# Performance work log

Hardware: AMD Instinct MI355X
Metric: run time of the kernel (lower is better)

The kernel has to match this reference:

```python
import math
import jax, jax.numpy as jnp
import numpy as np

B, S, D, H = 2, 4096, 512, 8
DH = D // H


def setup_inputs() -> dict:
    key = jax.random.key(0)
    ks = jax.random.split(key, 12)
    lim = 1.0 / math.sqrt(D)
    u = lambda k, shp: jax.random.uniform(k, shp, jnp.float32, -lim, lim)
    return {
        "x": jax.random.normal(ks[0], (B, S, D), jnp.float32),
        "gamma": jax.random.uniform(ks[1], (B, S, 1), jnp.float32),
        "Wq": u(ks[2], (D, D)), "bq": u(ks[3], (D,)),
        "Wk": u(ks[4], (D, D)), "bk": u(ks[5], (D,)),
        "Wv": u(ks[6], (D, D)), "bv": u(ks[7], (D,)),
        "Wo": u(ks[8], (D, D)), "bo": u(ks[9], (D,)),
    }


def reference(x, gamma, Wq, bq, Wk, bk, Wv, bv, Wo, bo):
    b, s, d = x.shape
    # projections (torch Linear: x @ W.T + b), split heads -> [B,H,S,DH]
    def proj(W, bias):
        return (x @ W.T + bias).reshape(b, s, H, DH).transpose(0, 2, 1, 3)
    q, k, v = proj(Wq, bq), proj(Wk, bk), proj(Wv, bv)

    scores = jnp.einsum("bhsd,bhtd->bhst", q, k) / math.sqrt(DH)  # [B,H,S,S]
    causal = jnp.triu(jnp.ones((s, s), bool), k=1)  # True above diagonal
    neg_inf = jnp.float32(-jnp.inf)
    scores = jnp.where(causal[None, None], neg_inf, scores)

    # hyperbolic positional bias: -log1p(gamma_i * max(i-j, 0) + 1e-8)
    pos = jnp.arange(s)
    delta = jnp.clip(pos[:, None] - pos[None, :], 0).astype(jnp.float32)  # [S,S]
    gamma_q = gamma[:, :, 0][:, :, None]  # [B,S,1]
    hyper = -jnp.log1p(gamma_q * delta + 1e-8)  # [B,S,S]
    hyper = jnp.where(causal[None], neg_inf, hyper)
    scores = scores + hyper[:, None]  # [B,H,S,S]

    attn = jax.nn.softmax(scores, axis=-1)
    out = jnp.einsum("bhst,bhtd->bhsd", attn, v)  # [B,H,S,DH]
    out = out.transpose(0, 2, 1, 3).reshape(b, s, d)
    return out @ Wo.T + bo
```

## Files before the change

### kernel.cpp

```cpp
#include <hip/hip_runtime.h>
#include <hip/hip_bf16.h>

#define Bb 2
#define Ss 4096
#define Dd 512
#define Hh 8
#define DHh 64

typedef __attribute__((ext_vector_type(8))) short short8;
typedef __attribute__((ext_vector_type(4))) float floatx4;

static __device__ __forceinline__ ushort bfbits(float f) {
  union { __hip_bfloat16 h; ushort u; } cv;
  cv.h = __float2bfloat16(f);
  return cv.u;
}

static __device__ __forceinline__ unsigned int packhi(float a, float b) {
  union { float f; unsigned int u; } ca, cb; ca.f = a; cb.f = b;
  return (ca.u >> 16) | (cb.u & 0xffff0000u);
}

__global__ void cvt_all(const float* __restrict__ x,
                        const float* __restrict__ w0, const float* __restrict__ w1,
                        const float* __restrict__ w2, const float* __restrict__ w3,
                        ushort* __restrict__ out) {
  const int XN4 = (Bb * Ss * Dd) / 4;
  const int WN4 = (Dd * Dd) / 4;
  int i = blockIdx.x * blockDim.x + threadIdx.x;
  if (i >= XN4 + 4 * WN4) return;
  const float* s; int li;
  if (i < XN4) { s = x; li = i; }
  else {
    int t = i - XN4; int j = t >> 16; li = t & (WN4 - 1);
    s = (j == 0) ? w0 : (j == 1) ? w1 : (j == 2) ? w2 : w3;
  }
  float4 f = ((const float4*)s)[li];
  ushort4 u;
  u.x = bfbits(f.x); u.y = bfbits(f.y); u.z = bfbits(f.z); u.w = bfbits(f.w);
  ((ushort4*)out)[i] = u;
}

static __device__ __forceinline__ int vperm(int s0) {
  int kb = (s0 >> 4) & 3, gq = (s0 >> 2) & 3;
  return (s0 & ~63) | ((kb >> 1) << 5) | (gq << 3) | ((kb & 1) << 2);
}

#define LDQK(buf, k0)                                                          \
  _Pragma("unroll")                                                            \
  for (int rb = 0; rb < 4; ++rb)                                               \
    af[buf][rb] = *(const short8*)(ap + (size_t)rb * 16 * 512 + (k0));         \
  _Pragma("unroll")                                                            \
  for (int cb = 0; cb < 4; ++cb)                                               \
    bf[buf][cb] = *(const short8*)(bp + (size_t)cb * 16 * 512 + (k0));

__global__ __launch_bounds__(256) void qkv_gemm(
    const ushort* __restrict__ xb,
    const ushort* __restrict__ Wq, const ushort* __restrict__ Wk, const ushort* __restrict__ Wv,
    const float* __restrict__ bq, const float* __restrict__ bk, const float* __restrict__ bv,
    ushort* __restrict__ qo, ushort* __restrict__ ko, ushort* __restrict__ vo)
{
  int mb = blockIdx.x / 12, rest = blockIdx.x % 12;
  int which = rest >> 2, nb = rest & 3;
  const ushort* Bw  = (which == 0) ? Wq : (which == 1) ? Wk : Wv;
  const float* bias = (which == 0) ? bq : (which == 1) ? bk : bv;
  int lane = threadIdx.x & 63, w = threadIdx.x >> 6;
  int wr = w & 1, wc = w >> 1;
  int g = lane >> 4, ln = lane & 15;
  int m0 = mb * 128 + wr * 64;
  int c0 = nb * 128 + wc * 64;
  const ushort* ap = xb + (size_t)(m0 + ln) * 512 + g * 8;
  const ushort* bp = Bw + (size_t)(c0 + ln) * 512 + g * 8;
  floatx4 acc[4][4] = {};
  short8 af[2][4], bf[2][4];
  LDQK(0, 0)
#pragma unroll
  for (int it = 0; it < 16; ++it) {
    int cur = it & 1;
    if (it < 15) { LDQK(cur ^ 1, (it + 1) * 32) }
#pragma unroll
    for (int rb = 0; rb < 4; ++rb)
#pragma unroll
      for (int cb = 0; cb < 4; ++cb)
        acc[rb][cb] = __builtin_amdgcn_mfma_f32_16x16x32_bf16(af[cur][rb], bf[cur][cb], acc[rb][cb], 0, 0, 0);
  }
  float scale = (which == 0) ? 0.18033688011112042f : 1.0f;
#pragma unroll
  for (int rb = 0; rb < 4; ++rb)
#pragma unroll
    for (int cb = 0; cb < 4; ++cb) {
      int col = c0 + cb * 16 + ln;
      float bv_ = bias[col];
      int hh = col >> 6, dh = col & 63;
      if (which == 2) {
        int i0 = m0 + rb * 16 + g * 4;
        int bI = i0 >> 12, s0 = i0 & (Ss - 1);
        ushort4 pk;
        pk.x = bfbits(acc[rb][cb][0] + bv_);
        pk.y = bfbits(acc[rb][cb][1] + bv_);
        pk.z = bfbits(acc[rb][cb][2] + bv_);
        pk.w = bfbits(acc[rb][cb][3] + bv_);
        *(ushort4*)(vo + (((size_t)bI * Hh + hh) * DHh + dh) * Ss + vperm(s0)) = pk;
      } else {
        ushort* outp = (which == 0) ? qo : ko;
#pragma unroll
        for (int r = 0; r < 4; ++r) {
          int i = m0 + rb * 16 + g * 4 + r;
          int bI = i >> 12, s = i & (Ss - 1);
          outp[(((size_t)bI * Hh + hh) * Ss + s) * DHh + dh] = bfbits((acc[rb][cb][r] + bv_) * scale);
        }
      }
    }
}

#define LD32(buf, k0)                                                          \
  af[buf][0] = *(const short8*)(ap + (k0));                                    \
  af[buf][1] = *(const short8*)(ap + 16 * 512 + (k0));                         \
  _Pragma("unroll")                                                            \
  for (int ns = 0; ns < 4; ++ns)                                               \
    bfr[buf][ns] = *(const short8*)(bp + (size_t)ns * 16 * 512 + (k0));

__global__ __launch_bounds__(256) void gemm_out(
    const ushort* __restrict__ A, const ushort* __restrict__ Bw,
    const float* __restrict__ bias, float* __restrict__ outp)
{
  int mb = blockIdx.x >> 3, nb = blockIdx.x & 7;
  int lane = threadIdx.x & 63, w = threadIdx.x >> 6;
  int g = lane >> 4, ln = lane & 15;
  int m0 = mb * 128 + w * 32;
  const ushort* ap = A + (size_t)(m0 + ln) * 512 + g * 8;
  const ushort* bp = Bw + (size_t)(nb * 64 + ln) * 512 + g * 8;
  floatx4 acc[2][4] = {};
  short8 af[2][2], bfr[2][4];
  LD32(0, 0)
#pragma unroll
  for (int it = 0; it < 16; ++it) {
    int cur = it & 1;
    if (it < 15) { LD32(cur ^ 1, (it + 1) * 32) }
#pragma unroll
    for (int ns = 0; ns < 4; ++ns) {
      acc[0][ns] = __builtin_amdgcn_mfma_f32_16x16x32_bf16(af[cur][0], bfr[cur][ns], acc[0][ns], 0, 0, 0);
      acc[1][ns] = __builtin_amdgcn_mfma_f32_16x16x32_bf16(af[cur][1], bfr[cur][ns], acc[1][ns], 0, 0, 0);
    }
  }
#pragma unroll
  for (int rb = 0; rb < 2; ++rb)
#pragma unroll
    for (int ns = 0; ns < 4; ++ns) {
      int col = nb * 64 + ns * 16 + ln;
      float bv_ = bias[col];
#pragma unroll
      for (int r = 0; r < 4; ++r)
        outp[(size_t)(m0 + rb * 16 + g * 4 + r) * 512 + col] = acc[rb][ns][r] + bv_;
    }
}

__global__ __launch_bounds__(192, 3) void flash13(
    const ushort* __restrict__ q, const ushort* __restrict__ k,
    const ushort* __restrict__ vt, const float* __restrict__ gamma,
    ushort* __restrict__ o)
{
  __shared__ __align__(16) float Pmrg[2][64][34];
  __shared__ __align__(16) ushort Tb[16 * 72];

  int z = blockIdx.x;
  int bh = z & 15;
  int b = bh >> 3, hh = bh & 7;
  int qsel = (z >> 4) & 1;
  int up = z >> 5;

  int tid = threadIdx.x;
  int wv = tid >> 6, lane = tid & 63;
  int g = lane >> 4, ln = lane & 15;

  const ushort* kp = k + ((size_t)bh * Ss + ln) * DHh + g * 8;
  const ushort* vp = vt + ((size_t)bh * DHh + ln) * Ss + g * 8;

#pragma unroll 1
  for (int rep = 0; rep < 2; ++rep) {
    int u = rep ? (63 - up) : up;
    int nkt = u + 1;
    int ktm = u;
    int qd = nkt / 3, rr = nkt % 3;
    int lo = wv * qd + (wv < rr ? wv : rr);
    int hi = lo + qd + (wv < rr ? 1 : 0);
    int q0 = (2 * u + qsel) * 32;

    const ushort* qp = q + ((size_t)bh * Ss + q0 + ln) * DHh + g * 8;
    short8 qf00 = *(const short8*)qp;
    short8 qf01 = *(const short8*)(qp + 32);
    short8 qf10 = *(const short8*)(qp + 16 * DHh);
    short8 qf11 = *(const short8*)(qp + 16 * DHh + 32);

    int qrow0 = q0 + ln, qrow1 = q0 + 16 + ln;
    float gm0 = gamma[(size_t)b * Ss + qrow0];
    float gm1 = gamma[(size_t)b * Ss + qrow1];
    float l2[2] = {0.0f, 0.0f};
    floatx4 oacc[2][4] = {};

    if (lo < hi) {
      short8 kfl[4], kfh[4];
      int kb0 = lo * 64;
#pragma unroll
      for (int ns = 0; ns < 4; ++ns) {
        kfl[ns] = *(const short8*)(kp + (size_t)(kb0 + ns * 16) * DHh);
        kfh[ns] = *(const short8*)(kp + (size_t)(kb0 + ns * 16) * DHh + 32);
      }

      for (int kt = lo; kt < hi; ++kt) {
        int kbase = kt * 64;
        bool last = (kt == ktm);
        short8 pfrag[2][2];
#pragma unroll
        for (int qb = 0; qb < 2; ++qb) {
          short8 qlo = qb ? qf10 : qf00;
          short8 qhi = qb ? qf11 : qf01;
          int qrow = qb ? qrow1 : qrow0;
          float gm = qb ? gm1 : gm0;
          int db = qrow - kbase - g * 4;
          float fd = (float)db;
          float base = fmaf(gm, fd, 1.0f);
#pragma unroll
          for (int nsg = 0; nsg < 2; ++nsg) {
            floatx4 za = {}, zb = {};
            za = __builtin_amdgcn_mfma_f32_16x16x32_bf16(kfl[2 * nsg + 0], qlo, za, 0, 0, 0);
            za = __builtin_amdgcn_mfma_f32_16x16x32_bf16(kfh[2 * nsg + 0], qhi, za, 0, 0, 0);
            zb = __builtin_amdgcn_mfma_f32_16x16x32_bf16(kfl[2 * nsg + 1], qlo, zb, 0, 0, 0);
            zb = __builtin_amdgcn_mfma_f32_16x16x32_bf16(kfh[2 * nsg + 1], qhi, zb, 0, 0, 0);
            float f[8];
#pragma unroll
            for (int r = 0; r < 4; ++r) { f[r] = za[r]; f[4 + r] = zb[r]; }
            float rs0 = 0.0f, rs1 = 0.0f;
            if (last) {
#pragma unroll
              for (int e = 0; e < 8; ++e) {
                int off = nsg * 32 + (e >> 2) * 16 + (e & 3);
                if (db - off < 0) f[e] = -1e30f;
                float delta = fmaxf(fd - (float)off, 0.0f);
                float wt = __builtin_amdgcn_rcpf(fmaf(gm, delta, 1.0f));
                float pv = __builtin_amdgcn_exp2f(f[e]) * wt;
                if (e & 1) rs1 += pv; else rs0 += pv;
                f[e] = pv;
              }
            } else {
#pragma unroll
              for (int e = 0; e < 8; ++e) {
                float off = (float)(nsg * 32 + (e >> 2) * 16 + (e & 3));
                float wt = __builtin_amdgcn_rcpf(fmaf(gm, -off, base));
                float pv = __builtin_amdgcn_exp2f(f[e]) * wt;
                if (e & 1) rs1 += pv; else rs0 += pv;
                f[e] = pv;
              }
            }
            l2[qb] += rs0 + rs1;
            uint4 pkd;
            pkd.x = packhi(f[0], f[1]);
            pkd.y = packhi(f[2], f[3]);
            pkd.z = packhi(f[4], f[5]);
            pkd.w = packhi(f[6], f[7]);
            pfrag[qb][nsg] = *(short8*)&pkd;
          }
        }
        if (kt + 1 < hi) {
          const ushort* kn = kp + (size_t)(kbase + 64) * DHh;
#pragma unroll
          for (int ns = 0; ns < 4; ++ns) {
            kfl[ns] = *(const short8*)(kn + (size_t)(ns * 16) * DHh);
            kfh[ns] = *(const short8*)(kn + (size_t)(ns * 16) * DHh + 32);
          }
        }
#pragma unroll
        for (int c = 0; c < 2; ++c) {
          short8 vfg[4];
#pragma unroll
          for (int ds = 0; ds < 4; ++ds)
            vfg[ds] = *(const short8*)(vp + (size_t)(ds * 16) * Ss + kbase + c * 32);
#pragma unroll
          for (int ds = 0; ds < 4; ++ds) {
            oacc[0][ds] = __builtin_amdgcn_mfma_f32_16x16x32_bf16(vfg[ds], pfrag[0][c], oacc[0][ds], 0, 0, 0);
            oacc[1][ds] = __builtin_amdgcn_mfma_f32_16x16x32_bf16(vfg[ds], pfrag[1][c], oacc[1][ds], 0, 0, 0);
          }
        }
      }
    }

    if (wv) {
#pragma unroll
      for (int qb = 0; qb < 2; ++qb)
#pragma unroll
        for (int ds = 0; ds < 4; ++ds)
#pragma unroll
          for (int r = 0; r < 4; ++r)
            Pmrg[wv - 1][lane][qb * 16 + ds * 4 + r] = oacc[qb][ds][r];
      Pmrg[wv - 1][lane][32] = l2[0];
      Pmrg[wv - 1][lane][33] = l2[1];
    }
    __syncthreads();
    if (wv == 0) {
#pragma unroll
      for (int qb = 0; qb < 2; ++qb) {
#pragma unroll
        for (int ds = 0; ds < 4; ++ds)
#pragma unroll
          for (int r = 0; r < 4; ++r)
            oacc[qb][ds][r] += Pmrg[0][lane][qb * 16 + ds * 4 + r]
                             + Pmrg[1][lane][qb * 16 + ds * 4 + r];
        float l = l2[qb] + Pmrg[0][lane][32 + qb] + Pmrg[1][lane][32 + qb];
        l += __shfl_xor(l, 16);
        l += __shfl_xor(l, 32);
        float linv = 1.0f / l;
        ushort* tb = &Tb[0];
#pragma unroll
        for (int ds = 0; ds < 4; ++ds)
#pragma unroll
          for (int r = 0; r < 4; ++r)
            tb[ln * 72 + ds * 16 + g * 4 + r] = bfbits(oacc[qb][ds][r] * linv);
        short8 v0 = *(const short8*)(tb + ln * 72 + g * 16);
        short8 v1 = *(const short8*)(tb + ln * 72 + g * 16 + 8);
        size_t oa = ((size_t)b * Ss + q0 + qb * 16 + ln) * Dd + hh * DHh + g * 16;
        *(short8*)(o + oa) = v0;
        *(short8*)(o + oa + 8) = v1;
      }
    }
    __syncthreads();
  }
}

extern "C" void kernel_launch(void* const* d_in, const int* in_sizes, int n_in,
                              void* d_out, int out_size, void* d_ws, size_t ws_size,
                              hipStream_t stream) {
  const float* x     = (const float*)d_in[0];
  const float* gamma = (const float*)d_in[1];
  const float* Wq    = (const float*)d_in[2];
  const float* bq    = (const float*)d_in[3];
  const float* Wk    = (const float*)d_in[4];
  const float* bk    = (const float*)d_in[5];
  const float* Wv    = (const float*)d_in[6];
  const float* bv    = (const float*)d_in[7];
  const float* Wo    = (const float*)d_in[8];
  const float* bo    = (const float*)d_in[9];

  const size_t NX = (size_t)Bb * Ss * Dd;
  const size_t NW = (size_t)Dd * Dd;
  ushort* xb  = (ushort*)d_ws;
  ushort* Wqb = xb + NX;
  ushort* Wkb = Wqb + NW;
  ushort* Wvb = Wkb + NW;
  ushort* Wob = Wvb + NW;
  ushort* qb  = Wob + NW;
  ushort* kb  = qb + NX;
  ushort* vtb = kb + NX;
  ushort* ab  = vtb + NX;

  const int total4 = (int)(NX / 4 + 4 * (NW / 4));
  cvt_all<<<(total4 + 255) / 256, 256, 0, stream>>>(x, Wq, Wk, Wv, Wo, xb);

  qkv_gemm<<<64 * 12, 256, 0, stream>>>(xb, Wqb, Wkb, Wvb, bq, bk, bv, qb, kb, vtb);

  flash13<<<1024, 192, 0, stream>>>(qb, kb, vtb, gamma, ab);

  gemm_out<<<512, 256, 0, stream>>>(ab, Wob, bo, (float*)d_out);
}
```

Baseline: 294.6 us.

## Shrink QKV GEMM tiles to one head per block and relax flash launch bounds

The QKV projection now assigns each block a 128-row by 64-column tile covering one head, with each of the four waves computing 32x64 instead of 64x64. The grid doubles to 1536 blocks for more parallelism and fewer registers per wave, at the cost of more redundant global loads of the weight tiles. The attention kernel also drops its min-blocks-per-CU hint, which lets the compiler use more registers but may lower occupancy.

```diff
diff --git a/kernel.cpp b/kernel.cpp
--- a/kernel.cpp
+++ b/kernel.cpp
@@ -46,10 +46,9 @@
   return (s0 & ~63) | ((kb >> 1) << 5) | (gq << 3) | ((kb & 1) << 2);
 }
 
-#define LDQK(buf, k0)                                                          \
-  _Pragma("unroll")                                                            \
-  for (int rb = 0; rb < 4; ++rb)                                               \
-    af[buf][rb] = *(const short8*)(ap + (size_t)rb * 16 * 512 + (k0));         \
+#define LDH(buf, k0)                                                           \
+  af[buf][0] = *(const short8*)(ap + (k0));                                    \
+  af[buf][1] = *(const short8*)(ap + 16 * 512 + (k0));                         \
   _Pragma("unroll")                                                            \
   for (int cb = 0; cb < 4; ++cb)                                               \
     bf[buf][cb] = *(const short8*)(bp + (size_t)cb * 16 * 512 + (k0));
@@ -60,38 +59,37 @@
     const float* __restrict__ bq, const float* __restrict__ bk, const float* __restrict__ bv,
     ushort* __restrict__ qo, ushort* __restrict__ ko, ushort* __restrict__ vo)
 {
-  int mb = blockIdx.x / 12, rest = blockIdx.x % 12;
-  int which = rest >> 2, nb = rest & 3;
+  int bid = blockIdx.x;
+  int hh = bid & 7, t = bid >> 3;
+  int which = t >> 6, mb = t & 63;
   const ushort* Bw  = (which == 0) ? Wq : (which == 1) ? Wk : Wv;
   const float* bias = (which == 0) ? bq : (which == 1) ? bk : bv;
   int lane = threadIdx.x & 63, w = threadIdx.x >> 6;
-  int wr = w & 1, wc = w >> 1;
   int g = lane >> 4, ln = lane & 15;
-  int m0 = mb * 128 + wr * 64;
-  int c0 = nb * 128 + wc * 64;
+  int m0 = mb * 128 + w * 32;
+  int c0 = hh * 64;
   const ushort* ap = xb + (size_t)(m0 + ln) * 512 + g * 8;
   const ushort* bp = Bw + (size_t)(c0 + ln) * 512 + g * 8;
-  floatx4 acc[4][4] = {};
-  short8 af[2][4], bf[2][4];
-  LDQK(0, 0)
+  floatx4 acc[2][4] = {};
+  short8 af[2][2], bf[2][4];
+  LDH(0, 0)
 #pragma unroll
   for (int it = 0; it < 16; ++it) {
     int cur = it & 1;
-    if (it < 15) { LDQK(cur ^ 1, (it + 1) * 32) }
-#pragma unroll
-    for (int rb = 0; rb < 4; ++rb)
-#pragma unroll
-      for (int cb = 0; cb < 4; ++cb)
-        acc[rb][cb] = __builtin_amdgcn_mfma_f32_16x16x32_bf16(af[cur][rb], bf[cur][cb], acc[rb][cb], 0, 0, 0);
+    if (it < 15) { LDH(cur ^ 1, (it + 1) * 32) }
+#pragma unroll
+    for (int cb = 0; cb < 4; ++cb) {
+      acc[0][cb] = __builtin_amdgcn_mfma_f32_16x16x32_bf16(af[cur][0], bf[cur][cb], acc[0][cb], 0, 0, 0);
+      acc[1][cb] = __builtin_amdgcn_mfma_f32_16x16x32_bf16(af[cur][1], bf[cur][cb], acc[1][cb], 0, 0, 0);
+    }
   }
   float scale = (which == 0) ? 0.18033688011112042f : 1.0f;
 #pragma unroll
-  for (int rb = 0; rb < 4; ++rb)
+  for (int rb = 0; rb < 2; ++rb)
 #pragma unroll
     for (int cb = 0; cb < 4; ++cb) {
-      int col = c0 + cb * 16 + ln;
-      float bv_ = bias[col];
-      int hh = col >> 6, dh = col & 63;
+      int dh = cb * 16 + ln;
+      float bv_ = bias[c0 + dh];
       if (which == 2) {
         int i0 = m0 + rb * 16 + g * 4;
         int bI = i0 >> 12, s0 = i0 & (Ss - 1);
@@ -155,7 +153,7 @@
     }
 }
 
-__global__ __launch_bounds__(192, 3) void flash13(
+__global__ __launch_bounds__(192) void flash14(
     const ushort* __restrict__ q, const ushort* __restrict__ k,
     const ushort* __restrict__ vt, const float* __restrict__ gamma,
     ushort* __restrict__ o)
@@ -355,9 +353,9 @@
   const int total4 = (int)(NX / 4 + 4 * (NW / 4));
   cvt_all<<<(total4 + 255) / 256, 256, 0, stream>>>(x, Wq, Wk, Wv, Wo, xb);
 
-  qkv_gemm<<<64 * 12, 256, 0, stream>>>(xb, Wqb, Wkb, Wvb, bq, bk, bv, qb, kb, vtb);
-
-  flash13<<<1024, 192, 0, stream>>>(qb, kb, vtb, gamma, ab);
+  qkv_gemm<<<1536, 256, 0, stream>>>(xb, Wqb, Wkb, Wvb, bq, bk, bv, qb, kb, vtb);
+
+  flash14<<<1024, 192, 0, stream>>>(qb, kb, vtb, gamma, ab);
 
   gemm_out<<<512, 256, 0, stream>>>(ab, Wob, bo, (float*)d_out);
 }
```

New measurement: 303.8 us. 1.03x slower.
